# Performance work log

Measured on AMD Instinct MI355X. Metric: run time of the kernel, lower is better.

Reference implementation:

```python
import jax, jax.numpy as jnp
import numpy as np

B, F, INP, S = 2048, 50, 2, 1024
LN_EPS = 1e-3
UPDATE_BIAS = -1.0
_TRUNC = 0.8796256610342398  # trunc-normal std correction from weight_init


def _std(fan_in, fan_out):
    return np.sqrt(2.0 / (fan_in + fan_out)) / _TRUNC


def setup_inputs() -> dict:
    key = jax.random.key(0)
    k_act, k_emb, k_gru, k_dec = jax.random.split(key, 4)
    return {
        "action": jax.random.normal(k_act, (B, F, INP), dtype=jnp.float32),
        "W_emb": jax.random.normal(k_emb, (INP, S), dtype=jnp.float32) * _std(INP, S),
        "W_gru": jax.random.normal(k_gru, (2 * S, 3 * S), dtype=jnp.float32) * _std(2 * S, 3 * S),
        "ln_gamma": jnp.ones((3 * S,), dtype=jnp.float32),
        "ln_beta": jnp.zeros((3 * S,), dtype=jnp.float32),
        "W_dec": jax.random.normal(k_dec, (S, INP), dtype=jnp.float32) * _std(S, INP),
        "b_dec": jnp.zeros((INP,), dtype=jnp.float32),
    }


def reference(action, W_emb, W_gru, ln_gamma, ln_beta, W_dec, b_dec):
    # action: [b, f, inp]
    emb = jnp.einsum("bfi,is->bfs", action, W_emb)  # [b, f, s]

    def step(prev, x_t):
        # prev, x_t: [b, s]
        parts = jnp.concatenate([x_t, prev], axis=-1) @ W_gru  # [b, 3s]
        mu = parts.mean(-1, keepdims=True)
        var = parts.var(-1, keepdims=True)
        parts = (parts - mu) / jnp.sqrt(var + LN_EPS) * ln_gamma + ln_beta
        reset, cand, update = jnp.split(parts, 3, axis=-1)
        reset = jax.nn.sigmoid(reset)
        cand = jnp.tanh(reset * cand)
        update = jax.nn.sigmoid(update + UPDATE_BIAS)
        h = update * cand + (1.0 - update) * prev
        return h, None

    prev0 = jnp.zeros_like(emb[:, 0])
    h_last, _ = jax.lax.scan(step, prev0, jnp.swapaxes(emb, 0, 1))  # scan over f
    outputs = h_last @ W_dec + b_dec  # [b, inp]
    return h_last[:, None], outputs[:, None]
```

## Files before the change

kernel.cpp:

```cpp
#include <hip/hip_runtime.h>

typedef unsigned short u16;
typedef unsigned int   u32;
typedef _Float16       f16;

#define B_SZ 2048
#define S_SZ 1024
#define N3   3072
#define F_SZ 50

typedef f16    f16x8 __attribute__((ext_vector_type(8)));
typedef float  f32x4 __attribute__((ext_vector_type(4)));
typedef u32    u32x4 __attribute__((ext_vector_type(4)));

__device__ __forceinline__ void glds16(const void* g, void* l) {
    __builtin_amdgcn_global_load_lds(
        (const __attribute__((address_space(1))) u32*)g,
        (__attribute__((address_space(3))) u32*)l, 16, 0, 0);
}

__global__ __launch_bounds__(256) void make_mx(
    const float* __restrict__ We, const float* __restrict__ Wg,
    float* __restrict__ Mx)
{
    int j  = blockIdx.x * 256 + threadIdx.x;
    int k0 = blockIdx.y * 64;
    float s0 = 0.f, s1 = 0.f;
    #pragma unroll 4
    for (int k = k0; k < k0 + 64; k++) {
        float w = Wg[(size_t)k * N3 + j];
        s0 += We[k] * w;
        s1 += We[S_SZ + k] * w;
    }
    atomicAdd(&Mx[j], s0);
    atomicAdd(&Mx[N3 + j], s1);
}

__global__ __launch_bounds__(256) void transpose_w(
    const float* __restrict__ Wg, f16* __restrict__ Wt)
{
    __shared__ float tile[32][33];
    int n0 = blockIdx.x * 32, k0 = blockIdx.y * 32;
    int c = threadIdx.x & 31, r = threadIdx.x >> 5;
    #pragma unroll
    for (int s = 0; s < 4; s++) {
        int rr = r + s * 8;
        tile[rr][c] = Wg[(size_t)(S_SZ + k0 + rr) * N3 + n0 + c];
    }
    __syncthreads();
    #pragma unroll
    for (int s = 0; s < 4; s++) {
        int rr = r + s * 8;
        Wt[(size_t)(n0 + rr) * S_SZ + k0 + c] = (f16)tile[c][rr];
    }
}

#define BM 128
#define BN 96
#define BK 64

__global__ __launch_bounds__(256, 2) void gemm_step(
    const f16* __restrict__ Wt,
    const f16* __restrict__ hh,
    const float* __restrict__ Mx,
    const float* __restrict__ act,
    f16* __restrict__ parts,
    int t)
{
    __shared__ __align__(16) f16 As[BM * BK];
    __shared__ __align__(16) f16 Bs[BN * BK];

    const int bid = blockIdx.x;
    const int xcd = bid & 7;
    const int loc = bid >> 3;
    const int mt  = (xcd & 1) * 8 + (loc & 7);
    const int nt  = (xcd >> 1) * 8 + (loc >> 3);
    const int m0  = mt * BM, n0 = nt * BN;

    const int tid  = threadIdx.x;
    const int lane = tid & 63;
    const int wave = tid >> 6;
    const int wr   = (wave >> 1) * 64;
    const int wc   = (wave & 1) * 48;
    const int quad = lane >> 4, lrow = lane & 15;
    const int swz  = (lrow & 7) * 8;

    const int lrow8 = lane >> 3;
    const int scolh = ((lane & 7) * 8) ^ (lrow8 * 8);

    f32x4 acc[4][3];
    #pragma unroll
    for (int i = 0; i < 4; i++)
        #pragma unroll
        for (int j = 0; j < 3; j++)
            acc[i][j] = (f32x4){0.f, 0.f, 0.f, 0.f};

    for (int kb = 0; kb < S_SZ; kb += BK) {
        __syncthreads();
        #pragma unroll
        for (int c = 0; c < 4; c++) {
            int ch  = wave * 4 + c;
            int row = ch * 8 + lrow8;
            glds16(&hh[(size_t)(m0 + row) * S_SZ + kb + scolh], &As[ch * 512]);
        }
        #pragma unroll
        for (int c = 0; c < 3; c++) {
            int ch  = wave * 3 + c;
            int row = ch * 8 + lrow8;
            glds16(&Wt[(size_t)(n0 + row) * S_SZ + kb + scolh], &Bs[ch * 512]);
        }
        __syncthreads();
        #pragma unroll
        for (int kk = 0; kk < 64; kk += 32) {
            f16x8 a[4], b[3];
            #pragma unroll
            for (int i = 0; i < 4; i++)
                a[i] = __builtin_bit_cast(f16x8,
                    *(const u32x4*)&As[(wr + i * 16 + lrow) * 64 +
                                       ((kk + quad * 8) ^ swz)]);
            #pragma unroll
            for (int j = 0; j < 3; j++)
                b[j] = __builtin_bit_cast(f16x8,
                    *(const u32x4*)&Bs[(wc + j * 16 + lrow) * 64 +
                                       ((kk + quad * 8) ^ swz)]);
            #pragma unroll
            for (int i = 0; i < 4; i++)
                #pragma unroll
                for (int j = 0; j < 3; j++)
                    acc[i][j] = __builtin_amdgcn_mfma_f32_16x16x32_f16(
                        a[i], b[j], acc[i][j], 0, 0, 0);
        }
    }

    float mx0[3], mx1[3];
    #pragma unroll
    for (int j = 0; j < 3; j++) {
        int n = n0 + wc + j * 16 + lrow;
        mx0[j] = Mx[n];
        mx1[j] = Mx[N3 + n];
    }
    #pragma unroll
    for (int i = 0; i < 4; i++) {
        #pragma unroll
        for (int rr = 0; rr < 4; rr++) {
            int m = m0 + wr + i * 16 + quad * 4 + rr;
            float a0 = act[((size_t)m * F_SZ + t) * 2 + 0];
            float a1 = act[((size_t)m * F_SZ + t) * 2 + 1];
            #pragma unroll
            for (int j = 0; j < 3; j++) {
                int n = n0 + wc + j * 16 + lrow;
                parts[(size_t)m * N3 + n] =
                    (f16)(acc[i][j][rr] + a0 * mx0[j] + a1 * mx1[j]);
            }
        }
    }
}

__global__ __launch_bounds__(256) void ln_gate_step(
    const f16* __restrict__ parts,
    const float* __restrict__ gamma,
    const float* __restrict__ beta,
    f16* __restrict__ hh,
    float* __restrict__ hout,
    int t)
{
    const int tid = threadIdx.x;
    const int r2  = tid >> 7;
    const int tl  = tid & 127;
    const int row = blockIdx.x * 2 + r2;
    const f16* p = parts + (size_t)row * N3 + tl * 8;

    float v[24];
    float s = 0.f, ss = 0.f;
    #pragma unroll
    for (int g = 0; g < 3; g++) {
        f16x8 x = *(const f16x8*)(p + g * S_SZ);
        #pragma unroll
        for (int e = 0; e < 8; e++) {
            float f = (float)x[e];
            v[g * 8 + e] = f;
            s += f; ss += f * f;
        }
    }
    #pragma unroll
    for (int o = 1; o < 64; o <<= 1) {
        s  += __shfl_xor(s, o);
        ss += __shfl_xor(ss, o);
    }
    __shared__ float red[8];
    int wave = tid >> 6, lane = tid & 63;
    if (lane == 0) { red[wave] = s; red[4 + wave] = ss; }
    __syncthreads();
    float S  = red[r2 * 2] + red[r2 * 2 + 1];
    float SS = red[4 + r2 * 2] + red[4 + r2 * 2 + 1];
    float mean = S * (1.f / N3);
    float var  = SS * (1.f / N3) - mean * mean;
    float rstd = rsqrtf(var + 1e-3f);

    float nv[24];
    #pragma unroll
    for (int g = 0; g < 3; g++) {
        f32x4 g0 = *(const f32x4*)(gamma + g * S_SZ + tl * 8);
        f32x4 g1 = *(const f32x4*)(gamma + g * S_SZ + tl * 8 + 4);
        f32x4 b0 = *(const f32x4*)(beta  + g * S_SZ + tl * 8);
        f32x4 b1 = *(const f32x4*)(beta  + g * S_SZ + tl * 8 + 4);
        #pragma unroll
        for (int e = 0; e < 4; e++) {
            nv[g * 8 + e]     = (v[g * 8 + e]     - mean) * rstd * g0[e] + b0[e];
            nv[g * 8 + e + 4] = (v[g * 8 + e + 4] - mean) * rstd * g1[e] + b1[e];
        }
    }

    size_t hbase = (size_t)row * S_SZ + tl * 8;
    f16x8 hp = *(const f16x8*)(hh + hbase);
    f16x8 hs;
    f32x4 ho0, ho1;
    #pragma unroll
    for (int e = 0; e < 8; e++) {
        float rg = 1.f / (1.f + __expf(-nv[e]));
        float x  = rg * nv[8 + e];
        float tt = __expf(-2.f * fabsf(x));
        float cg = __builtin_copysignf((1.f - tt) / (1.f + tt), x);
        float ug = 1.f / (1.f + __expf(-(nv[16 + e] - 1.f)));
        float hv = ug * cg + (1.f - ug) * (float)hp[e];
        hs[e] = (f16)hv;
        if (e < 4) ho0[e] = hv; else ho1[e - 4] = hv;
    }
    *(f16x8*)(hh + hbase) = hs;
    if (t == F_SZ - 1) {
        *(f32x4*)(hout + hbase)     = ho0;
        *(f32x4*)(hout + hbase + 4) = ho1;
    }
}

__global__ __launch_bounds__(256) void final_out(
    const float* __restrict__ h, const float* __restrict__ Wd,
    const float* __restrict__ bd, float* __restrict__ out)
{
    int row = blockIdx.x * 4 + (threadIdx.x >> 6);
    int lane = threadIdx.x & 63;
    const float* hr = h + (size_t)row * S_SZ;
    float s0 = 0.f, s1 = 0.f;
    #pragma unroll
    for (int k = lane; k < S_SZ; k += 64) {
        float x = hr[k];
        s0 += x * Wd[k * 2];
        s1 += x * Wd[k * 2 + 1];
    }
    #pragma unroll
    for (int o = 32; o > 0; o >>= 1) {
        s0 += __shfl_down(s0, o);
        s1 += __shfl_down(s1, o);
    }
    if (lane == 0) {
        out[(size_t)B_SZ * S_SZ + row * 2 + 0] = s0 + bd[0];
        out[(size_t)B_SZ * S_SZ + row * 2 + 1] = s1 + bd[1];
    }
}

extern "C" void kernel_launch(void* const* d_in, const int* in_sizes, int n_in,
                              void* d_out, int out_size, void* d_ws, size_t ws_size,
                              hipStream_t stream)
{
    const float* act = (const float*)d_in[0];
    const float* We  = (const float*)d_in[1];
    const float* Wg  = (const float*)d_in[2];
    const float* lng = (const float*)d_in[3];
    const float* lnb = (const float*)d_in[4];
    const float* Wd  = (const float*)d_in[5];
    const float* bd  = (const float*)d_in[6];
    float* out = (float*)d_out;

    char* ws = (char*)d_ws;
    f16*   Wt    = (f16*)ws;
    float* Mx    = (float*)(ws + 6291456);
    f16*   hh    = (f16*)(ws + 6316032);
    f16*   parts = (f16*)(ws + 10510336);

    hipMemsetAsync(hh, 0, (size_t)B_SZ * S_SZ * 2, stream);
    hipMemsetAsync(Mx, 0, 2 * N3 * 4, stream);
    make_mx<<<dim3(N3 / 256, 16), 256, 0, stream>>>(We, Wg, Mx);
    transpose_w<<<dim3(N3 / 32, S_SZ / 32), 256, 0, stream>>>(Wg, Wt);

    for (int t = 0; t < F_SZ; t++) {
        gemm_step<<<dim3(512), 256, 0, stream>>>(Wt, hh, Mx, act, parts, t);
        ln_gate_step<<<B_SZ / 2, 256, 0, stream>>>(parts, lng, lnb, hh, out, t);
    }
    final_out<<<B_SZ / 4, 256, 0, stream>>>(out, Wd, bd, out);
}
```

Before: 1.559 ms.

## Store weights and hidden state in MFMA fragment layout and load directly to registers

Weights and the recurrent hidden state are stored in a pre-tiled layout that matches the MFMA operand fragments. The GEMM can then load A/B operands straight from global memory into registers with double-buffering and no LDS staging or barriers. Each wave now computes a 64x96 tile with 256 blocks at occupancy 1, where before it was 512 blocks with LDS tiles. This removes LDS traffic and syncs, at the cost of more register pressure, fewer resident waves, and reuse that now depends on L2 rather than LDS.

```diff
diff --git a/kernel.cpp b/kernel.cpp
--- a/kernel.cpp
+++ b/kernel.cpp
@@ -8,16 +8,12 @@
 #define S_SZ 1024
 #define N3   3072
 #define F_SZ 50
+#define NK   32
 
 typedef f16    f16x8 __attribute__((ext_vector_type(8)));
 typedef float  f32x4 __attribute__((ext_vector_type(4)));
 typedef u32    u32x4 __attribute__((ext_vector_type(4)));
 
-__device__ __forceinline__ void glds16(const void* g, void* l) {
-    __builtin_amdgcn_global_load_lds(
-        (const __attribute__((address_space(1))) u32*)g,
-        (__attribute__((address_space(3))) u32*)l, 16, 0, 0);
-}
 
 __global__ __launch_bounds__(256) void make_mx(
     const float* __restrict__ We, const float* __restrict__ Wg,
@@ -37,7 +33,7 @@
 }
 
 __global__ __launch_bounds__(256) void transpose_w(
-    const float* __restrict__ Wg, f16* __restrict__ Wt)
+    const float* __restrict__ Wg, f16* __restrict__ WtF)
 {
     __shared__ float tile[32][33];
     int n0 = blockIdx.x * 32, k0 = blockIdx.y * 32;
@@ -51,91 +47,82 @@
     #pragma unroll
     for (int s = 0; s < 4; s++) {
         int rr = r + s * 8;
-        Wt[(size_t)(n0 + rr) * S_SZ + k0 + c] = (f16)tile[c][rr];
-    }
-}
-
-#define BM 128
-#define BN 96
-#define BK 64
-
-__global__ __launch_bounds__(256, 2) void gemm_step(
-    const f16* __restrict__ Wt,
-    const f16* __restrict__ hh,
+        int n = n0 + rr, k = k0 + c;
+        size_t o = ((size_t)(n >> 4) * NK + (k >> 5)) * 512
+                 + (((k >> 3) & 3) * 16 + (n & 15)) * 8 + (k & 7);
+        WtF[o] = (f16)tile[c][rr];
+    }
+}
+
+__global__ __launch_bounds__(256, 1) void gemm_step(
+    const f16* __restrict__ WtF,
+    const f16* __restrict__ hhF,
     const float* __restrict__ Mx,
     const float* __restrict__ act,
     f16* __restrict__ parts,
     int t)
 {
-    __shared__ __align__(16) f16 As[BM * BK];
-    __shared__ __align__(16) f16 Bs[BN * BK];
-
-    const int bid = blockIdx.x;
-    const int xcd = bid & 7;
-    const int loc = bid >> 3;
-    const int mt  = (xcd & 1) * 8 + (loc & 7);
-    const int nt  = (xcd >> 1) * 8 + (loc >> 3);
-    const int m0  = mt * BM, n0 = nt * BN;
-
-    const int tid  = threadIdx.x;
-    const int lane = tid & 63;
-    const int wave = tid >> 6;
-    const int wr   = (wave >> 1) * 64;
-    const int wc   = (wave & 1) * 48;
+    const int bid  = blockIdx.x;
+    const int xcd  = bid & 7, idx = bid >> 3;
+    const int mt   = (xcd & 3) * 4 + (idx & 3);
+    const int nt   = (xcd >> 2) * 8 + (idx >> 2);
+    const int lane = threadIdx.x & 63;
+    const int wave = threadIdx.x >> 6;
+    const int m0   = mt * 128 + (wave >> 1) * 64;
+    const int n0   = nt * 192 + (wave & 1) * 96;
+    const int R0   = m0 >> 4;
+    const int C0   = n0 >> 4;
     const int quad = lane >> 4, lrow = lane & 15;
-    const int swz  = (lrow & 7) * 8;
-
-    const int lrow8 = lane >> 3;
-    const int scolh = ((lane & 7) * 8) ^ (lrow8 * 8);
-
-    f32x4 acc[4][3];
+
+    const f16* Ab = hhF + (size_t)R0 * NK * 512 + lane * 8;
+    const f16* Bb = WtF + (size_t)C0 * NK * 512 + lane * 8;
+
+    f32x4 acc[4][6];
     #pragma unroll
     for (int i = 0; i < 4; i++)
         #pragma unroll
-        for (int j = 0; j < 3; j++)
+        for (int j = 0; j < 6; j++)
             acc[i][j] = (f32x4){0.f, 0.f, 0.f, 0.f};
 
-    for (int kb = 0; kb < S_SZ; kb += BK) {
-        __syncthreads();
-        #pragma unroll
-        for (int c = 0; c < 4; c++) {
-            int ch  = wave * 4 + c;
-            int row = ch * 8 + lrow8;
-            glds16(&hh[(size_t)(m0 + row) * S_SZ + kb + scolh], &As[ch * 512]);
-        }
-        #pragma unroll
-        for (int c = 0; c < 3; c++) {
-            int ch  = wave * 3 + c;
-            int row = ch * 8 + lrow8;
-            glds16(&Wt[(size_t)(n0 + row) * S_SZ + kb + scolh], &Bs[ch * 512]);
-        }
-        __syncthreads();
-        #pragma unroll
-        for (int kk = 0; kk < 64; kk += 32) {
-            f16x8 a[4], b[3];
+    f16x8 A0[4], A1[4], B0[6], B1[6];
+
+    auto lda = [&](f16x8* A, int kb) {
+        #pragma unroll
+        for (int i = 0; i < 4; i++)
+            A[i] = __builtin_bit_cast(f16x8,
+                *(const u32x4*)(Ab + ((i * NK + kb) << 9)));
+    };
+    auto ldb = [&](f16x8* Bv, int kb) {
+        #pragma unroll
+        for (int j = 0; j < 6; j++)
+            Bv[j] = __builtin_bit_cast(f16x8,
+                *(const u32x4*)(Bb + ((j * NK + kb) << 9)));
+    };
+
+    lda(A0, 0); ldb(B0, 0);
+    lda(A1, 1); ldb(B1, 1);
+
+    for (int kb2 = 0; kb2 < NK / 2; kb2++) {
+        #pragma unroll
+        for (int i = 0; i < 4; i++)
             #pragma unroll
-            for (int i = 0; i < 4; i++)
-                a[i] = __builtin_bit_cast(f16x8,
-                    *(const u32x4*)&As[(wr + i * 16 + lrow) * 64 +
-                                       ((kk + quad * 8) ^ swz)]);
+            for (int j = 0; j < 6; j++)
+                acc[i][j] = __builtin_amdgcn_mfma_f32_16x16x32_f16(
+                    A0[i], B0[j], acc[i][j], 0, 0, 0);
+        if (kb2 < NK / 2 - 1) { lda(A0, 2 * kb2 + 2); ldb(B0, 2 * kb2 + 2); }
+        #pragma unroll
+        for (int i = 0; i < 4; i++)
             #pragma unroll
-            for (int j = 0; j < 3; j++)
-                b[j] = __builtin_bit_cast(f16x8,
-                    *(const u32x4*)&Bs[(wc + j * 16 + lrow) * 64 +
-                                       ((kk + quad * 8) ^ swz)]);
-            #pragma unroll
-            for (int i = 0; i < 4; i++)
-                #pragma unroll
-                for (int j = 0; j < 3; j++)
-                    acc[i][j] = __builtin_amdgcn_mfma_f32_16x16x32_f16(
-                        a[i], b[j], acc[i][j], 0, 0, 0);
-        }
-    }
-
-    float mx0[3], mx1[3];
-    #pragma unroll
-    for (int j = 0; j < 3; j++) {
-        int n = n0 + wc + j * 16 + lrow;
+            for (int j = 0; j < 6; j++)
+                acc[i][j] = __builtin_amdgcn_mfma_f32_16x16x32_f16(
+                    A1[i], B1[j], acc[i][j], 0, 0, 0);
+        if (kb2 < NK / 2 - 1) { lda(A1, 2 * kb2 + 3); ldb(B1, 2 * kb2 + 3); }
+    }
+
+    float mx0[6], mx1[6];
+    #pragma unroll
+    for (int j = 0; j < 6; j++) {
+        int n = n0 + j * 16 + lrow;
         mx0[j] = Mx[n];
         mx1[j] = Mx[N3 + n];
     }
@@ -143,12 +130,12 @@
     for (int i = 0; i < 4; i++) {
         #pragma unroll
         for (int rr = 0; rr < 4; rr++) {
-            int m = m0 + wr + i * 16 + quad * 4 + rr;
+            int m = m0 + i * 16 + quad * 4 + rr;
             float a0 = act[((size_t)m * F_SZ + t) * 2 + 0];
             float a1 = act[((size_t)m * F_SZ + t) * 2 + 1];
             #pragma unroll
-            for (int j = 0; j < 3; j++) {
-                int n = n0 + wc + j * 16 + lrow;
+            for (int j = 0; j < 6; j++) {
+                int n = n0 + j * 16 + lrow;
                 parts[(size_t)m * N3 + n] =
                     (f16)(acc[i][j][rr] + a0 * mx0[j] + a1 * mx1[j]);
             }
@@ -211,8 +198,9 @@
         }
     }
 
-    size_t hbase = (size_t)row * S_SZ + tl * 8;
-    f16x8 hp = *(const f16x8*)(hh + hbase);
+    size_t hfrag = ((size_t)(row >> 4) * NK + (tl >> 2)) * 512
+                 + ((size_t)((tl & 3) * 16 + (row & 15))) * 8;
+    f16x8 hp = *(const f16x8*)(hh + hfrag);
     f16x8 hs;
     f32x4 ho0, ho1;
     #pragma unroll
@@ -226,8 +214,9 @@
         hs[e] = (f16)hv;
         if (e < 4) ho0[e] = hv; else ho1[e - 4] = hv;
     }
-    *(f16x8*)(hh + hbase) = hs;
+    *(f16x8*)(hh + hfrag) = hs;
     if (t == F_SZ - 1) {
+        size_t hbase = (size_t)row * S_SZ + tl * 8;
         *(f32x4*)(hout + hbase)     = ho0;
         *(f32x4*)(hout + hbase + 4) = ho1;
     }
@@ -283,7 +272,7 @@
     transpose_w<<<dim3(N3 / 32, S_SZ / 32), 256, 0, stream>>>(Wg, Wt);
 
     for (int t = 0; t < F_SZ; t++) {
-        gemm_step<<<dim3(512), 256, 0, stream>>>(Wt, hh, Mx, act, parts, t);
+        gemm_step<<<dim3(256), 256, 0, stream>>>(Wt, hh, Mx, act, parts, t);
         ln_gate_step<<<B_SZ / 2, 256, 0, stream>>>(parts, lng, lnb, hh, out, t);
     }
     final_out<<<B_SZ / 4, 256, 0, stream>>>(out, Wd, bd, out);
```

Measured after the change: 1.679 ms. 7.7% more time.
